# Kernel tuning notes

Hardware: AMD Instinct MI355X
Metric: run time of the kernel (lower is better)

Reference implementation:

```python
import jax, jax.numpy as jnp
import numpy as np

N = 50000      # amino-acid nodes
DIN = 64       # input feature dim
DH = 64        # hidden dim (= GAT out_feats per head)
H = 4          # attention heads
E_RES, E_SEQ, E_KNN = 400000, 100000, 400000
EPS = 1e-5


def setup_inputs() -> dict:
    key = jax.random.key(0)
    ks = iter(jax.random.split(key, 32))
    def nrm(shape, scale=0.1):
        return jax.random.normal(next(ks), shape, dtype=jnp.float32) * scale
    def edges(E):
        s = jax.random.randint(next(ks), (E,), 0, N, dtype=jnp.int32)
        d = jax.random.randint(next(ks), (E,), 0, N, dtype=jnp.int32)
        return s, d
    x = nrm((N, DIN), 1.0)
    src_res, dst_res = edges(E_RES)
    src_seq, dst_seq = edges(E_SEQ)
    src_knn, dst_knn = edges(E_KNN)
    inp = dict(x=x, src_res=src_res, dst_res=dst_res, src_seq=src_seq,
               dst_seq=dst_seq, src_knn=src_knn, dst_knn=dst_knn)
    # layer 0 (in=DIN), layer 1 (in=DH): per-relation stacked GAT params
    inp.update(W0=nrm((3, DIN, H * DH)), al0=nrm((3, H, DH)), ar0=nrm((3, H, DH)),
               b0=nrm((3, H * DH)), rW0=nrm((3, DIN, H * DH)))
    inp.update(W1=nrm((3, DH, H * DH)), al1=nrm((3, H, DH)), ar1=nrm((3, H, DH)),
               b1=nrm((3, H * DH)), rW1=nrm((3, DH, H * DH)))
    inp.update(fcW0=nrm((DH, DH)), fcb0=nrm((DH,)), fcW1=nrm((DH, DH)), fcb1=nrm((DH,)))
    inp.update(g0=jnp.ones((DIN,), jnp.float32), be0=jnp.zeros((DIN,), jnp.float32),
               g1=jnp.ones((DH,), jnp.float32), be1=jnp.zeros((DH,), jnp.float32))
    return inp


def _bn(x, g, b):
    mu = jnp.mean(x, axis=0)
    var = jnp.mean((x - mu) ** 2, axis=0)
    return (x - mu) * jax.lax.rsqrt(var + EPS) * g + b


def _gat(h, src, dst, W, al, ar, bias, rW):
    # DGL GATConv (feat_drop off in eval, residual=True via res_fc Linear, bias)
    n = h.shape[0]
    fs = (h @ W).reshape(n, H, DH)                    # [N,H,D]
    el = jnp.sum(fs * al, axis=-1)                    # [N,H]
    er = jnp.sum(fs * ar, axis=-1)
    e = jax.nn.leaky_relu(el[src] + er[dst], 0.2)     # [E,H]
    m = jax.ops.segment_max(e, dst, num_segments=n)
    a = jnp.exp(e - m[dst])
    s = jax.ops.segment_sum(a, dst, num_segments=n)
    alpha = a / s[dst]                                # edge-softmax per dst/head
    rst = jax.ops.segment_sum(alpha[:, :, None] * fs[src], dst, num_segments=n)
    return rst + (h @ rW).reshape(n, H, DH) + bias.reshape(1, H, DH)


def _layer(x, edges, W, al, ar, b, rW, fcW, fcb, g, be):
    x = _bn(x, g, be)
    h = jnp.zeros((x.shape[0], H, DH), x.dtype)
    for r, (s_, d_) in enumerate(edges):              # 3 relation types, summed
        h = h + _gat(x, s_, d_, W[r], al[r], ar[r], b[r], rW[r])
    x = jnp.mean(h, axis=1)                           # mean over heads
    return jax.nn.relu(x @ fcW + fcb)


def reference(x, src_res, dst_res, src_seq, dst_seq, src_knn, dst_knn,
              W0, al0, ar0, b0, rW0, W1, al1, ar1, b1, rW1,
              fcW0, fcb0, fcW1, fcb1, g0, be0, g1, be1):
    edges = [(src_res, dst_res), (src_seq, dst_seq), (src_knn, dst_knn)]
    x = _layer(x, edges, W0, al0, ar0, b0, rW0, fcW0, fcb0, g0, be0)
    x = _layer(x, edges, W1, al1, ar1, b1, rW1, fcW1, fcb1, g1, be1)
    return x
```

## Files before the change

### kernel.cpp

```cpp
#include <hip/hip_runtime.h>
#include <math.h>

#define NN    50000
#define DD    64
#define HH    4
#define E_RES 400000
#define E_SEQ 100000
#define E_KNN 400000
#define ETOT  (E_RES+E_SEQ+E_KNN)
#define SCH   4096
#define SNB   ((NN + SCH - 1)/SCH)
#define RPS   (NN + 4)
#define MBLK  ((NN+63)/64)
#define NBLK  ((NN+255)/256)
#define ZS    800
#define KTOT  864
#define CTPS  (ETOT + 32)
#define NGRP  (NN/4)
#define AGB   ((3*NGRP)/4)

typedef __attribute__((ext_vector_type(8))) short short8;
typedef __attribute__((ext_vector_type(4))) float floatx4;

__device__ inline unsigned short f2bf(float f){
  union{float f; unsigned u;} v; v.f=f;
  unsigned r = v.u + 0x7FFF + ((v.u>>16)&1);
  return (unsigned short)(r>>16);
}
__device__ inline float bf2f(unsigned short u){
  union{unsigned u; float f;} v; v.u=(unsigned)u<<16; return v.f;
}

__global__ void k_hist3(const int* __restrict__ d0, const int* __restrict__ d1,
                        const int* __restrict__ d2, int* __restrict__ cnt){
  int i = blockIdx.x*256 + threadIdx.x;
  if(i < E_RES)                atomicAdd(&cnt[d0[i]], 1);
  else if(i < E_RES+E_SEQ)     atomicAdd(&cnt[NN + d1[i-E_RES]], 1);
  else if(i < ETOT)            atomicAdd(&cnt[2*NN + d2[i-E_RES-E_SEQ]], 1);
}

__global__ void __launch_bounds__(256)
k_blocksum(const int* __restrict__ hist, int* __restrict__ bsums){
  int r = blockIdx.x / SNB, b = blockIdx.x % SNB;
  const int* cnt = hist + r*NN;
  int t = threadIdx.x;
  int end = min((b+1)*SCH, NN);
  int s = 0;
  for(int j = b*SCH + t; j < end; j += 256) s += cnt[j];
  __shared__ int sh[4];
  for(int off=32; off; off>>=1) s += __shfl_down(s, off, 64);
  int lane = t & 63, w = t >> 6;
  if(lane==0) sh[w]=s;
  __syncthreads();
  if(t==0) bsums[blockIdx.x] = sh[0]+sh[1]+sh[2]+sh[3];
}

__global__ void __launch_bounds__(256)
k_scanwrite(const int* __restrict__ hist, const int* __restrict__ bsums,
            int* __restrict__ rowptr, int* __restrict__ cursor){
  int r = blockIdx.x / SNB, b = blockIdx.x % SNB;
  const int* cnt = hist + r*NN;
  int* rp  = rowptr + r*RPS;
  int* cur = cursor + r*NN;
  __shared__ int sh_off;
  __shared__ int wtot[4];
  int t = threadIdx.x;
  if(t==0){
    int o=0, tot=0;
    for(int i=0;i<SNB;i++){ int v=bsums[r*SNB+i]; if(i<b) o+=v; tot+=v; }
    sh_off=o;
    if(b==0) rp[NN]=tot;
  }
  int base = b*SCH + t*16;
  int v[16];
  bool full = (base+16 <= NN);
  if(full){
    int4 a0=((const int4*)cnt)[base/4+0];
    int4 a1=((const int4*)cnt)[base/4+1];
    int4 a2=((const int4*)cnt)[base/4+2];
    int4 a3=((const int4*)cnt)[base/4+3];
    v[0]=a0.x;v[1]=a0.y;v[2]=a0.z;v[3]=a0.w;
    v[4]=a1.x;v[5]=a1.y;v[6]=a1.z;v[7]=a1.w;
    v[8]=a2.x;v[9]=a2.y;v[10]=a2.z;v[11]=a2.w;
    v[12]=a3.x;v[13]=a3.y;v[14]=a3.z;v[15]=a3.w;
  } else {
    for(int j=0;j<16;j++){ int idx=base+j; v[j]=(idx<NN)?cnt[idx]:0; }
  }
  int loc=0;
  #pragma unroll
  for(int j=0;j<16;j++) loc += v[j];
  int lane = t & 63, w = t >> 6;
  int inc = loc;
  for(int off=1; off<64; off<<=1){ int n=__shfl_up(inc, off, 64); if(lane>=off) inc+=n; }
  if(lane==63) wtot[w]=inc;
  __syncthreads();
  int woff=0;
  for(int i=0;i<w;i++) woff += wtot[i];
  int run = sh_off + woff + inc - loc;
  if(full){
    int o[16];
    #pragma unroll
    for(int j=0;j<16;j++){ o[j]=run; run+=v[j]; }
    ((int4*)rp )[base/4+0]=make_int4(o[0],o[1],o[2],o[3]);
    ((int4*)rp )[base/4+1]=make_int4(o[4],o[5],o[6],o[7]);
    ((int4*)rp )[base/4+2]=make_int4(o[8],o[9],o[10],o[11]);
    ((int4*)rp )[base/4+3]=make_int4(o[12],o[13],o[14],o[15]);
    ((int4*)cur)[base/4+0]=make_int4(o[0],o[1],o[2],o[3]);
    ((int4*)cur)[base/4+1]=make_int4(o[4],o[5],o[6],o[7]);
    ((int4*)cur)[base/4+2]=make_int4(o[8],o[9],o[10],o[11]);
    ((int4*)cur)[base/4+3]=make_int4(o[12],o[13],o[14],o[15]);
  } else {
    for(int j=0;j<16;j++){
      int idx=base+j;
      if(idx<NN){ rp[idx]=run; cur[idx]=run; run+=v[j]; }
    }
  }
}

__global__ void k_scatter3(const int* __restrict__ s0, const int* __restrict__ d0,
                           const int* __restrict__ s1, const int* __restrict__ d1,
                           const int* __restrict__ s2, const int* __restrict__ d2,
                           int* __restrict__ cursor, int* __restrict__ csr){
  int i = blockIdx.x*256 + threadIdx.x;
  if(i < E_RES){
    int pos = atomicAdd(&cursor[d0[i]],1);
    __builtin_nontemporal_store(s0[i], &csr[pos]);
  } else if(i < E_RES+E_SEQ){
    int j=i-E_RES;
    int pos = atomicAdd(&cursor[NN+d1[j]],1);
    __builtin_nontemporal_store(s1[j], &csr[E_RES+pos]);
  } else if(i < ETOT){
    int j=i-E_RES-E_SEQ;
    int pos = atomicAdd(&cursor[2*NN+d2[j]],1);
    __builtin_nontemporal_store(s2[j], &csr[E_RES+E_SEQ+pos]);
  }
}

__global__ void k_bnstats(const float* __restrict__ x, float* __restrict__ stats,
                          unsigned short* __restrict__ Abf){
  __shared__ float sh[512];
  int t = threadIdx.x, col = t & 63, rg = t >> 6;
  float s=0.f, q=0.f;
  for(int row = blockIdx.x*4 + rg; row < NN; row += gridDim.x*4){
    float v = x[(size_t)row*64 + col]; s += v; q += v*v;
    Abf[(size_t)row*64 + col] = f2bf(v);
  }
  sh[t]=s; sh[256+t]=q; __syncthreads();
  if(rg==0){
    s = sh[col]+sh[64+col]+sh[128+col]+sh[192+col];
    q = sh[256+col]+sh[320+col]+sh[384+col]+sh[448+col];
    atomicAdd(&stats[col], s); atomicAdd(&stats[64+col], q);
  }
}

__global__ void __launch_bounds__(256)
k_prep3(const float* __restrict__ stats, const float* __restrict__ g,
        const float* __restrict__ be, const float* __restrict__ W,
        const float* __restrict__ al, const float* __restrict__ ar,
        const float* __restrict__ b, const float* __restrict__ rW,
        const float* __restrict__ fcW, const float* __restrict__ fcb,
        float* __restrict__ wbufF){
  __shared__ float scale[64], shift[64];
  int t = threadIdx.x;
  if(t<64){
    float mu  = stats[t]*(1.0f/NN);
    float var = stats[64+t]*(1.0f/NN) - mu*mu;
    float sc  = g[t]*rsqrtf(var + 1e-5f);
    scale[t]=sc; shift[t]=be[t]-mu*sc;
  }
  __syncthreads();
  char* wb = (char*)wbufF;
  unsigned short* Wf = (unsigned short*)wbufF;
  float* biasF = (float*)(wb + 110592);
  int bid = blockIdx.x;
  if(bid < 52){
    __shared__ float fcWs[4096];
    for(int i=t;i<4096;i+=256) fcWs[i]=fcW[i];
    __syncthreads();
    int j = bid*16 + (t>>4);
    int cg = (t&15)*4;
    float Wrow[64];
    if(j < 64){
      for(int d=0; d<64; d++){
        float w=0.f;
        for(int r=0;r<3;r++)
          #pragma unroll
          for(int h=0;h<4;h++)
            w += rW[((size_t)(r*64+j))*256 + h*64 + d];
        Wrow[d] = scale[j]*0.25f*w;
      }
    } else {
      int jj = j-64;
      int r = jj>>8, dc = jj&255, h = dc&3, c = dc>>2;
      const float* Wp = W + ((size_t)(r*64+c))*256 + h*64;
      float sc = 0.25f*scale[c];
      #pragma unroll
      for(int d=0; d<64; d++) Wrow[d] = sc*Wp[d];
    }
    #pragma unroll
    for(int cc=0; cc<4; cc++){
      int col = cg+cc;
      float acc=0.f;
      #pragma unroll
      for(int d=0; d<64; d++) acc += Wrow[d]*fcWs[d*64+col];
      Wf[(size_t)col*KTOT + j] = f2bf(acc);
    }
  } else if(bid < 58){
    int wv = (bid-52)*4 + (t>>6);
    int r = wv >> 3, cc = wv & 7, h = cc & 3, k = t & 63;
    const float* av = ((cc>=4)?ar:al) + (r*HH+h)*64;
    const float* Wk = W + ((size_t)(r*64+k))*256 + h*64;
    float w=0.f;
    for(int d2=0; d2<64; d2++) w += Wk[d2]*av[d2];
    float* WelR = (float*)(wb + 110848 + r*2080);
    WelR[cc*64 + k] = scale[k]*w;
    float bp = shift[k]*w;
    for(int off=32; off; off>>=1) bp += __shfl_down(bp, off, 64);
    if(k==0) (WelR + 512)[cc] = bp;
  } else {
    __shared__ float S[3][64];
    __shared__ float BH[64];
    if(t<192){
      int r=t>>6, d=t&63;
      float s=0.f;
      #pragma unroll
      for(int h=0;h<4;h++){
        const float* Wp = W + (size_t)(r*64)*256 + h*64 + d;
        for(int k=0;k<64;k++) s += shift[k]*Wp[(size_t)k*256];
      }
      S[r][d]=0.25f*s;
    } else {
      int d = t-192;
      float s=0.f;
      for(int k=0;k<64;k++){
        float w=0.f;
        for(int r=0;r<3;r++)
          #pragma unroll
          for(int h=0;h<4;h++)
            w += rW[((size_t)(r*64+k))*256 + h*64 + d];
        s += shift[k]*0.25f*w;
      }
      float bb=0.f;
      for(int r=0;r<3;r++)
        #pragma unroll
        for(int h=0;h<4;h++) bb += b[r*256 + h*64 + d];
      BH[d] = s + 0.25f*bb;
    }
    __syncthreads();
    if(t<192){
      int r=t>>6, col=t&63;
      float acc=0.f;
      for(int d=0;d<64;d++) acc += S[r][d]*fcW[d*64+col];
      Wf[(size_t)col*KTOT + 832 + r] = f2bf(acc);
    } else {
      int col=t-192;
      float acc=0.f;
      for(int d=0;d<64;d++) acc += BH[d]*fcW[d*64+col];
      biasF[col] = acc + fcb[col];
    }
    if(t<64){
      for(int j=835;j<KTOT;j++) Wf[(size_t)t*KTOT + j] = 0;
    }
  }
}

__global__ void __launch_bounds__(256)
k_el3(const float* __restrict__ A, const float* __restrict__ wbufF,
      float* __restrict__ EL){
  int r = blockIdx.x / NBLK;
  const char* wb = (const char*)wbufF;
  const float* Wel = (const float*)(wb + 110848 + r*2080);
  const float* biasE = Wel + 512;
  float* ELr = EL + (size_t)r*NN*8;
  __shared__ float sw[512];
  __shared__ float sb[8];
  int t = threadIdx.x;
  sw[t]=Wel[t]; sw[256+t]=Wel[256+t];
  if(t<8) sb[t]=biasE[t];
  __syncthreads();
  int n = (blockIdx.x % NBLK)*256 + t;
  if(n>=NN) return;
  float acc[8];
  #pragma unroll
  for(int c=0;c<8;c++) acc[c]=sb[c];
  const float4* Ar = (const float4*)(A + (size_t)n*64);
  #pragma unroll
  for(int kq=0;kq<16;kq++){
    float4 a = Ar[kq];
    #pragma unroll
    for(int c=0;c<8;c++){
      const float* w = sw + c*64 + kq*4;
      acc[c] += a.x*w[0] + a.y*w[1] + a.z*w[2] + a.w*w[3];
    }
  }
  ((float4*)ELr)[n*2]   = make_float4(acc[0],acc[1],acc[2],acc[3]);
  ((float4*)ELr)[n*2+1] = make_float4(acc[4],acc[5],acc[6],acc[7]);
}

__global__ void __launch_bounds__(256)
k_edgecoef3(const float* __restrict__ EL, const int* __restrict__ rowptr,
            const int* __restrict__ csr, unsigned short* __restrict__ coefT){
  int r = blockIdx.x / NBLK;
  const float* ELr = EL + (size_t)r*NN*8;
  const int* rp = rowptr + r*RPS;
  int off = (r==0)?0:(r==1)?E_RES:(E_RES+E_SEQ);
  const int* cs = csr + off;
  unsigned short* t0 = coefT + off;
  unsigned short* t1 = coefT + (size_t)CTPS + off;
  unsigned short* t2 = coefT + (size_t)2*CTPS + off;
  unsigned short* t3 = coefT + (size_t)3*CTPS + off;
  int n = (blockIdx.x % NBLK)*256 + threadIdx.x;
  if(n>=NN) return;
  int beg = rp[n], end = rp[n+1];
  if(end<=beg) return;
  const float4 er = ((const float4*)ELr)[n*2+1];
  float m0=-1e30f,m1=-1e30f,m2=-1e30f,m3=-1e30f;
  float s0=0.f,s1=0.f,s2=0.f,s3=0.f;
  for(int i=beg;i<end;i++){
    int src = cs[i];
    float4 el = ((const float4*)ELr)[src*2];
    float e0=el.x+er.x, e1=el.y+er.y, e2=el.z+er.z, e3=el.w+er.w;
    e0 = e0>0.f? e0 : 0.2f*e0;
    e1 = e1>0.f? e1 : 0.2f*e1;
    e2 = e2>0.f? e2 : 0.2f*e2;
    e3 = e3>0.f? e3 : 0.2f*e3;
    float n0=fmaxf(m0,e0); s0=s0*__expf(m0-n0)+__expf(e0-n0); m0=n0;
    float n1=fmaxf(m1,e1); s1=s1*__expf(m1-n1)+__expf(e1-n1); m1=n1;
    float n2=fmaxf(m2,e2); s2=s2*__expf(m2-n2)+__expf(e2-n2); m2=n2;
    float n3=fmaxf(m3,e3); s3=s3*__expf(m3-n3)+__expf(e3-n3); m3=n3;
  }
  float r0=1.f/s0, r1=1.f/s1, r2=1.f/s2, r3=1.f/s3;
  for(int i=beg;i<end;i++){
    int src = cs[i];
    float4 el = ((const float4*)ELr)[src*2];
    float e0=el.x+er.x, e1=el.y+er.y, e2=el.z+er.z, e3=el.w+er.w;
    e0 = e0>0.f? e0 : 0.2f*e0;
    e1 = e1>0.f? e1 : 0.2f*e1;
    e2 = e2>0.f? e2 : 0.2f*e2;
    e3 = e3>0.f? e3 : 0.2f*e3;
    t0[i] = f2bf(__expf(e0-m0)*r0);
    t1[i] = f2bf(__expf(e1-m1)*r1);
    t2[i] = f2bf(__expf(e2-m2)*r2);
    t3[i] = f2bf(__expf(e3-m3)*r3);
  }
}

__global__ void __launch_bounds__(256)
k_aggzr(const unsigned short* __restrict__ Abf, const int* __restrict__ rowptr,
        const int* __restrict__ csr, const unsigned short* __restrict__ coefT,
        unsigned short* __restrict__ Zbf){
  int w    = blockIdx.x*4 + (threadIdx.x>>6);
  int lane = threadIdx.x & 63;
  int r = w / NGRP;
  int g = w - r*NGRP;
  int n4 = g << 2;
  int m = lane & 15, kq = lane >> 4;
  int nn = m >> 2, h = m & 3;
  const int* rp = rowptr + r*RPS;
  int off = (r==0)?0:(r==1)?E_RES:(E_RES+E_SEQ);
  const int* cs = csr + off;
  const unsigned short* cT = coefT + (size_t)h*CTPS + off;
  int rpn  = rp[n4+nn];
  int rpn1 = rp[n4+nn+1];
  unsigned dg = (unsigned)(rpn1 - rpn);
  int beg = __shfl(rpn, 0, 64);
  int end = __shfl(rpn1, 15, 64);
  floatx4 acc0={0.f,0.f,0.f,0.f};
  floatx4 acc1={0.f,0.f,0.f,0.f};
  floatx4 acc2={0.f,0.f,0.f,0.f};
  floatx4 acc3={0.f,0.f,0.f,0.f};
  for(int eb = (beg & ~31); eb < end; eb += 32){
    int p0 = eb + kq*8;
    union { uint4 q; short8 v; } af;
    af.q = *(const uint4*)(cT + p0);
    int qd = p0 - rpn;
    unsigned w0 = (((unsigned)(qd+0)<dg)?0x0000FFFFu:0u) | (((unsigned)(qd+1)<dg)?0xFFFF0000u:0u);
    unsigned w1 = (((unsigned)(qd+2)<dg)?0x0000FFFFu:0u) | (((unsigned)(qd+3)<dg)?0xFFFF0000u:0u);
    unsigned w2 = (((unsigned)(qd+4)<dg)?0x0000FFFFu:0u) | (((unsigned)(qd+5)<dg)?0xFFFF0000u:0u);
    unsigned w3 = (((unsigned)(qd+6)<dg)?0x0000FFFFu:0u) | (((unsigned)(qd+7)<dg)?0xFFFF0000u:0u);
    af.q.x &= w0; af.q.y &= w1; af.q.z &= w2; af.q.w &= w3;
    const int* csp = cs + p0;
    int s0=csp[0],s1=csp[1],s2=csp[2],s3=csp[3],s4=csp[4],s5=csp[5],s6=csp[6],s7=csp[7];
    const unsigned short* q0 = Abf + ((size_t)s0<<6) + m;
    const unsigned short* q1 = Abf + ((size_t)s1<<6) + m;
    const unsigned short* q2 = Abf + ((size_t)s2<<6) + m;
    const unsigned short* q3 = Abf + ((size_t)s3<<6) + m;
    const unsigned short* q4 = Abf + ((size_t)s4<<6) + m;
    const unsigned short* q5 = Abf + ((size_t)s5<<6) + m;
    const unsigned short* q6 = Abf + ((size_t)s6<<6) + m;
    const unsigned short* q7 = Abf + ((size_t)s7<<6) + m;
    union { unsigned u[4]; short8 v; } b0,b1,b2,b3;
    b0.u[0]=(unsigned)q0[0] |((unsigned)q1[0]<<16);
    b0.u[1]=(unsigned)q2[0] |((unsigned)q3[0]<<16);
    b0.u[2]=(unsigned)q4[0] |((unsigned)q5[0]<<16);
    b0.u[3]=(unsigned)q6[0] |((unsigned)q7[0]<<16);
    b1.u[0]=(unsigned)q0[16]|((unsigned)q1[16]<<16);
    b1.u[1]=(unsigned)q2[16]|((unsigned)q3[16]<<16);
    b1.u[2]=(unsigned)q4[16]|((unsigned)q5[16]<<16);
    b1.u[3]=(unsigned)q6[16]|((unsigned)q7[16]<<16);
    b2.u[0]=(unsigned)q0[32]|((unsigned)q1[32]<<16);
    b2.u[1]=(unsigned)q2[32]|((unsigned)q3[32]<<16);
    b2.u[2]=(unsigned)q4[32]|((unsigned)q5[32]<<16);
    b2.u[3]=(unsigned)q6[32]|((unsigned)q7[32]<<16);
    b3.u[0]=(unsigned)q0[48]|((unsigned)q1[48]<<16);
    b3.u[1]=(unsigned)q2[48]|((unsigned)q3[48]<<16);
    b3.u[2]=(unsigned)q4[48]|((unsigned)q5[48]<<16);
    b3.u[3]=(unsigned)q6[48]|((unsigned)q7[48]<<16);
    acc0 = __builtin_amdgcn_mfma_f32_16x16x32_bf16(af.v, b0.v, acc0, 0,0,0);
    acc1 = __builtin_amdgcn_mfma_f32_16x16x32_bf16(af.v, b1.v, acc1, 0,0,0);
    acc2 = __builtin_amdgcn_mfma_f32_16x16x32_bf16(af.v, b2.v, acc2, 0,0,0);
    acc3 = __builtin_amdgcn_mfma_f32_16x16x32_bf16(af.v, b3.v, acc3, 0,0,0);
  }
  size_t zb = (size_t)(n4 + kq)*ZS + (size_t)r*256 + (size_t)m*4;
  ushort4 o;
  o.x=f2bf(acc0[0]); o.y=f2bf(acc0[1]); o.z=f2bf(acc0[2]); o.w=f2bf(acc0[3]);
  *(ushort4*)(Zbf + zb)       = o;
  o.x=f2bf(acc1[0]); o.y=f2bf(acc1[1]); o.z=f2bf(acc1[2]); o.w=f2bf(acc1[3]);
  *(ushort4*)(Zbf + zb + 64)  = o;
  o.x=f2bf(acc2[0]); o.y=f2bf(acc2[1]); o.z=f2bf(acc2[2]); o.w=f2bf(acc2[3]);
  *(ushort4*)(Zbf + zb + 128) = o;
  o.x=f2bf(acc3[0]); o.y=f2bf(acc3[1]); o.z=f2bf(acc3[2]); o.w=f2bf(acc3[3]);
  *(ushort4*)(Zbf + zb + 192) = o;
  int degk = __shfl((int)dg, kq<<2, 64);
  size_t fb = (size_t)(n4+kq)*ZS + 768;
  if(m==0)
    Zbf[fb + r] = degk>0 ? (unsigned short)0x3F80 : (unsigned short)0;
  if(r==0 && m>=1){
    Zbf[fb + 2 + m] = 0;
    if(m<15) Zbf[fb + 17 + m] = 0;
  }
}

__global__ void __launch_bounds__(256)
k_mfmaZ(const unsigned short* __restrict__ Abf, const unsigned short* __restrict__ Zbf,
        const float* __restrict__ wbufF, float* __restrict__ out,
        unsigned short* __restrict__ Abf2, float* __restrict__ stats, int dostats){
  __shared__ float spart[4][2][32];
  const unsigned short* Wf = (const unsigned short*)wbufF;
  const float* biasF = (const float*)((const char*)wbufF + 110592);
  int t = threadIdx.x, wv = t>>6, lane = t&63, m = lane&15, kq = lane>>4;
  int rt = blockIdx.x >> 1, ch = blockIdx.x & 1;
  int cb = ch*2;
  int row = rt*64 + wv*16 + m;
  int rc = row < NN ? row : NN-1;
  floatx4 acc0 = {0.f,0.f,0.f,0.f};
  floatx4 acc1 = {0.f,0.f,0.f,0.f};
  const unsigned short* Arow = Abf + (size_t)rc*64;
  const unsigned short* Zrow = Zbf + (size_t)rc*ZS;
  #pragma unroll
  for(int kb=0; kb<27; kb++){
    short8 a;
    if(kb<2) a = *(const short8*)(Arow + kb*32 + kq*8);
    else     a = *(const short8*)(Zrow + (kb-2)*32 + kq*8);
    int ko = kb*32 + kq*8;
    short8 b0 = *(const short8*)(Wf + (size_t)((cb+0)*16+m)*KTOT + ko);
    short8 b1 = *(const short8*)(Wf + (size_t)((cb+1)*16+m)*KTOT + ko);
    acc0 = __builtin_amdgcn_mfma_f32_16x16x32_bf16(a, b0, acc0, 0,0,0);
    acc1 = __builtin_amdgcn_mfma_f32_16x16x32_bf16(a, b1, acc1, 0,0,0);
  }
  int orow = rt*64 + wv*16 + kq*4;
  #pragma unroll
  for(int ct=0; ct<2; ct++){
    int col = (cb+ct)*16 + m;
    int lcol = ct*16 + m;
    floatx4 acc = (ct==0)?acc0:acc1;
    float bb = biasF[col];
    float sv=0.f, qv=0.f;
    #pragma unroll
    for(int ri=0; ri<4; ri++){
      int ro = orow + ri;
      if(ro < NN){
        float v = fmaxf(acc[ri] + bb, 0.f);
        out[(size_t)ro*64 + col] = v;
        if(dostats){
          Abf2[(size_t)ro*64 + col] = f2bf(v);
          sv += v; qv += v*v;
        }
      }
    }
    if(dostats){
      sv += __shfl_xor(sv, 16, 64); qv += __shfl_xor(qv, 16, 64);
      sv += __shfl_xor(sv, 32, 64); qv += __shfl_xor(qv, 32, 64);
      if(kq==0){ spart[wv][0][lcol]=sv; spart[wv][1][lcol]=qv; }
    }
  }
  if(dostats){
    __syncthreads();
    if(t<32){
      float s = spart[0][0][t]+spart[1][0][t]+spart[2][0][t]+spart[3][0][t];
      float q = spart[0][1][t]+spart[1][1][t]+spart[2][1][t]+spart[3][1][t];
      atomicAdd(&stats[ch*32+t], s); atomicAdd(&stats[64+ch*32+t], q);
    }
  }
}

extern "C" void kernel_launch(void* const* d_in, const int* in_sizes, int n_in,
                              void* d_out, int out_size, void* d_ws, size_t ws_size,
                              hipStream_t stream){
  const float* x      =(const float*)d_in[0];
  const int* src_res  =(const int*)d_in[1];
  const int* dst_res  =(const int*)d_in[2];
  const int* src_seq  =(const int*)d_in[3];
  const int* dst_seq  =(const int*)d_in[4];
  const int* src_knn  =(const int*)d_in[5];
  const int* dst_knn  =(const int*)d_in[6];
  const float* W0 =(const float*)d_in[7];
  const float* al0=(const float*)d_in[8];
  const float* ar0=(const float*)d_in[9];
  const float* b0 =(const float*)d_in[10];
  const float* rW0=(const float*)d_in[11];
  const float* W1 =(const float*)d_in[12];
  const float* al1=(const float*)d_in[13];
  const float* ar1=(const float*)d_in[14];
  const float* b1 =(const float*)d_in[15];
  const float* rW1=(const float*)d_in[16];
  const float* fcW0=(const float*)d_in[17];
  const float* fcb0=(const float*)d_in[18];
  const float* fcW1=(const float*)d_in[19];
  const float* fcb1=(const float*)d_in[20];
  const float* g0 =(const float*)d_in[21];
  const float* be0=(const float*)d_in[22];
  const float* g1 =(const float*)d_in[23];
  const float* be1=(const float*)d_in[24];

  char* ws=(char*)d_ws;
  int*   hist   =(int*)  (ws+0);
  float* stats0 =(float*)(ws+600000);
  float* stats1 =(float*)(ws+600512);
  int*   rowptr =(int*)  (ws+601024);
  int*   cursor =(int*)  (ws+1201088);
  int*   csr    =(int*)  (ws+1801088);
  float* wbuf   =(float*)(ws+5401088);
  int*   bsums  =(int*)  (ws+5525344);
  unsigned short* Abf  =(unsigned short*)(ws+5526528);
  unsigned short* Zbf  =(unsigned short*)(ws+11926528UL);
  float* xbuf   =(float*)(ws+91926528UL);
  float* EL     =(float*)(ws+104726528UL);
  unsigned short* coefT=(unsigned short*)(ws+109526528UL);
  unsigned short* Abf2 =(unsigned short*)(ws+123926528UL);

  hipMemsetAsync(ws, 0, 601024, stream);

  const int EBLK=(ETOT+255)/256;
  k_hist3<<<EBLK,256,0,stream>>>(dst_res,dst_seq,dst_knn,hist);
  k_blocksum<<<3*SNB,256,0,stream>>>(hist,bsums);
  k_scanwrite<<<3*SNB,256,0,stream>>>(hist,bsums,rowptr,cursor);
  k_scatter3<<<EBLK,256,0,stream>>>(src_res,dst_res,src_seq,dst_seq,
                                    src_knn,dst_knn,cursor,csr);

  k_bnstats<<<256,256,0,stream>>>(x,stats0,Abf);
  k_prep3<<<59,256,0,stream>>>(stats0,g0,be0,W0,al0,ar0,b0,rW0,fcW0,fcb0,wbuf);
  k_el3<<<3*NBLK,256,0,stream>>>(x,wbuf,EL);
  k_edgecoef3<<<3*NBLK,256,0,stream>>>(EL,rowptr,csr,coefT);
  k_aggzr<<<AGB,256,0,stream>>>(Abf,rowptr,csr,coefT,Zbf);
  k_mfmaZ<<<2*MBLK,256,0,stream>>>(Abf,Zbf,wbuf,xbuf,Abf2,stats1,1);
  k_prep3<<<59,256,0,stream>>>(stats1,g1,be1,W1,al1,ar1,b1,rW1,fcW1,fcb1,wbuf);
  k_el3<<<3*NBLK,256,0,stream>>>(xbuf,wbuf,EL);
  k_edgecoef3<<<3*NBLK,256,0,stream>>>(EL,rowptr,csr,coefT);
  k_aggzr<<<AGB,256,0,stream>>>(Abf2,rowptr,csr,coefT,Zbf);
  k_mfmaZ<<<2*MBLK,256,0,stream>>>(Abf2,Zbf,wbuf,(float*)d_out,Abf2,stats0,0);
}
```

Baseline: 510.0 us.

## Build CSR via two-level bucket partition with shared-memory atomics

Replaces the per-node global-atomic histogram, scan and scatter with a two-pass bucket sort. Edges are first counted and partitioned into coarse 512-node buckets per relation using shared-memory counters. Each bucket is then locally histogrammed, scanned and scattered in shared memory to produce rowptr and csr. This aims to cut contended global atomics and random global writes during CSR construction. The cost is an extra packed-pairs pass through a buffer that aliases Zbf, and it relies on src and rank values fitting in 16 bits.

```diff
diff --git a/kernel.cpp b/kernel.cpp
--- a/kernel.cpp
+++ b/kernel.cpp
@@ -8,8 +8,6 @@
 #define E_SEQ 100000
 #define E_KNN 400000
 #define ETOT  (E_RES+E_SEQ+E_KNN)
-#define SCH   4096
-#define SNB   ((NN + SCH - 1)/SCH)
 #define RPS   (NN + 4)
 #define MBLK  ((NN+63)/64)
 #define NBLK  ((NN+255)/256)
@@ -18,6 +16,10 @@
 #define CTPS  (ETOT + 32)
 #define NGRP  (NN/4)
 #define AGB   ((3*NGRP)/4)
+#define NBUK  98
+#define TBUK  (3*NBUK)
+#define EPB   4096
+#define PABLK ((ETOT+EPB-1)/EPB)
 
 typedef __attribute__((ext_vector_type(8))) short short8;
 typedef __attribute__((ext_vector_type(4))) float floatx4;
@@ -31,108 +33,118 @@
   union{unsigned u; float f;} v; v.u=(unsigned)u<<16; return v.f;
 }
 
-__global__ void k_hist3(const int* __restrict__ d0, const int* __restrict__ d1,
-                        const int* __restrict__ d2, int* __restrict__ cnt){
-  int i = blockIdx.x*256 + threadIdx.x;
-  if(i < E_RES)                atomicAdd(&cnt[d0[i]], 1);
-  else if(i < E_RES+E_SEQ)     atomicAdd(&cnt[NN + d1[i-E_RES]], 1);
-  else if(i < ETOT)            atomicAdd(&cnt[2*NN + d2[i-E_RES-E_SEQ]], 1);
-}
-
-__global__ void __launch_bounds__(256)
-k_blocksum(const int* __restrict__ hist, int* __restrict__ bsums){
-  int r = blockIdx.x / SNB, b = blockIdx.x % SNB;
-  const int* cnt = hist + r*NN;
+
+__global__ void __launch_bounds__(256)
+k_bucketcnt(const int* __restrict__ d0, const int* __restrict__ d1,
+            const int* __restrict__ d2, int* __restrict__ bcnt){
+  __shared__ int cnt[TBUK];
   int t = threadIdx.x;
-  int end = min((b+1)*SCH, NN);
-  int s = 0;
-  for(int j = b*SCH + t; j < end; j += 256) s += cnt[j];
-  __shared__ int sh[4];
-  for(int off=32; off; off>>=1) s += __shfl_down(s, off, 64);
-  int lane = t & 63, w = t >> 6;
-  if(lane==0) sh[w]=s;
-  __syncthreads();
-  if(t==0) bsums[blockIdx.x] = sh[0]+sh[1]+sh[2]+sh[3];
-}
-
-__global__ void __launch_bounds__(256)
-k_scanwrite(const int* __restrict__ hist, const int* __restrict__ bsums,
-            int* __restrict__ rowptr, int* __restrict__ cursor){
-  int r = blockIdx.x / SNB, b = blockIdx.x % SNB;
-  const int* cnt = hist + r*NN;
-  int* rp  = rowptr + r*RPS;
-  int* cur = cursor + r*NN;
-  __shared__ int sh_off;
-  __shared__ int wtot[4];
+  for(int i=t;i<TBUK;i+=256) cnt[i]=0;
+  __syncthreads();
+  int ebase = blockIdx.x*EPB;
+  #pragma unroll
+  for(int j=0;j<16;j++){
+    int i = ebase + j*256 + t;
+    int d, r;
+    if(i < E_RES){ d=d0[i]; r=0; }
+    else if(i < E_RES+E_SEQ){ d=d1[i-E_RES]; r=1; }
+    else if(i < ETOT){ d=d2[i-E_RES-E_SEQ]; r=2; }
+    else continue;
+    atomicAdd(&cnt[r*NBUK + (d>>9)], 1);
+  }
+  __syncthreads();
+  for(int i=t;i<TBUK;i+=256){ int c=cnt[i]; if(c) atomicAdd(&bcnt[i], c); }
+}
+
+__global__ void k_bucketscan(const int* __restrict__ bcnt,
+                             int* __restrict__ bbase, int* __restrict__ bcur){
+  __shared__ int sh[TBUK];
   int t = threadIdx.x;
-  if(t==0){
-    int o=0, tot=0;
-    for(int i=0;i<SNB;i++){ int v=bsums[r*SNB+i]; if(i<b) o+=v; tot+=v; }
-    sh_off=o;
-    if(b==0) rp[NN]=tot;
-  }
-  int base = b*SCH + t*16;
-  int v[16];
-  bool full = (base+16 <= NN);
-  if(full){
-    int4 a0=((const int4*)cnt)[base/4+0];
-    int4 a1=((const int4*)cnt)[base/4+1];
-    int4 a2=((const int4*)cnt)[base/4+2];
-    int4 a3=((const int4*)cnt)[base/4+3];
-    v[0]=a0.x;v[1]=a0.y;v[2]=a0.z;v[3]=a0.w;
-    v[4]=a1.x;v[5]=a1.y;v[6]=a1.z;v[7]=a1.w;
-    v[8]=a2.x;v[9]=a2.y;v[10]=a2.z;v[11]=a2.w;
-    v[12]=a3.x;v[13]=a3.y;v[14]=a3.z;v[15]=a3.w;
-  } else {
-    for(int j=0;j<16;j++){ int idx=base+j; v[j]=(idx<NN)?cnt[idx]:0; }
-  }
-  int loc=0;
-  #pragma unroll
-  for(int j=0;j<16;j++) loc += v[j];
-  int lane = t & 63, w = t >> 6;
-  int inc = loc;
-  for(int off=1; off<64; off<<=1){ int n=__shfl_up(inc, off, 64); if(lane>=off) inc+=n; }
-  if(lane==63) wtot[w]=inc;
-  __syncthreads();
-  int woff=0;
-  for(int i=0;i<w;i++) woff += wtot[i];
-  int run = sh_off + woff + inc - loc;
-  if(full){
-    int o[16];
-    #pragma unroll
-    for(int j=0;j<16;j++){ o[j]=run; run+=v[j]; }
-    ((int4*)rp )[base/4+0]=make_int4(o[0],o[1],o[2],o[3]);
-    ((int4*)rp )[base/4+1]=make_int4(o[4],o[5],o[6],o[7]);
-    ((int4*)rp )[base/4+2]=make_int4(o[8],o[9],o[10],o[11]);
-    ((int4*)rp )[base/4+3]=make_int4(o[12],o[13],o[14],o[15]);
-    ((int4*)cur)[base/4+0]=make_int4(o[0],o[1],o[2],o[3]);
-    ((int4*)cur)[base/4+1]=make_int4(o[4],o[5],o[6],o[7]);
-    ((int4*)cur)[base/4+2]=make_int4(o[8],o[9],o[10],o[11]);
-    ((int4*)cur)[base/4+3]=make_int4(o[12],o[13],o[14],o[15]);
-  } else {
-    for(int j=0;j<16;j++){
-      int idx=base+j;
-      if(idx<NN){ rp[idx]=run; cur[idx]=run; run+=v[j]; }
-    }
-  }
-}
-
-__global__ void k_scatter3(const int* __restrict__ s0, const int* __restrict__ d0,
-                           const int* __restrict__ s1, const int* __restrict__ d1,
-                           const int* __restrict__ s2, const int* __restrict__ d2,
-                           int* __restrict__ cursor, int* __restrict__ csr){
-  int i = blockIdx.x*256 + threadIdx.x;
-  if(i < E_RES){
-    int pos = atomicAdd(&cursor[d0[i]],1);
-    __builtin_nontemporal_store(s0[i], &csr[pos]);
-  } else if(i < E_RES+E_SEQ){
-    int j=i-E_RES;
-    int pos = atomicAdd(&cursor[NN+d1[j]],1);
-    __builtin_nontemporal_store(s1[j], &csr[E_RES+pos]);
-  } else if(i < ETOT){
-    int j=i-E_RES-E_SEQ;
-    int pos = atomicAdd(&cursor[2*NN+d2[j]],1);
-    __builtin_nontemporal_store(s2[j], &csr[E_RES+E_SEQ+pos]);
+  if(t < 64){
+    int carry = 0;
+    for(int c=0;c<5;c++){
+      int idx = c*64 + t;
+      int v = (idx < TBUK) ? bcnt[idx] : 0;
+      int inc = v;
+      for(int off=1; off<64; off<<=1){ int n=__shfl_up(inc, off, 64); if(t>=off) inc+=n; }
+      if(idx < TBUK) sh[idx] = carry + inc - v;
+      carry += __shfl(inc, 63, 64);
+    }
+  }
+  __syncthreads();
+  if(t < TBUK){ bbase[t] = sh[t]; bcur[t] = sh[t]; }
+  if(t == 0) bbase[TBUK] = ETOT;
+}
+
+__global__ void __launch_bounds__(256)
+k_partA(const int* __restrict__ s0, const int* __restrict__ d0,
+        const int* __restrict__ s1, const int* __restrict__ d1,
+        const int* __restrict__ s2, const int* __restrict__ d2,
+        int* __restrict__ bcur, unsigned* __restrict__ pairs){
+  __shared__ int cnt[TBUK];
+  __shared__ int gb[TBUK];
+  int t = threadIdx.x;
+  for(int i=t;i<TBUK;i+=256) cnt[i]=0;
+  __syncthreads();
+  int ebase = blockIdx.x*EPB;
+  unsigned meta[16], pk[16];
+  #pragma unroll
+  for(int j=0;j<16;j++){
+    int i = ebase + j*256 + t;
+    int s, d, r;
+    if(i < E_RES){ s=s0[i]; d=d0[i]; r=0; }
+    else if(i < E_RES+E_SEQ){ int k=i-E_RES; s=s1[k]; d=d1[k]; r=1; }
+    else if(i < ETOT){ int k=i-E_RES-E_SEQ; s=s2[k]; d=d2[k]; r=2; }
+    else { meta[j]=0xFFFFFFFFu; continue; }
+    int bk = r*NBUK + (d>>9);
+    int rk = atomicAdd(&cnt[bk], 1);
+    meta[j] = ((unsigned)bk<<16) | (unsigned)rk;
+    pk[j]   = ((unsigned)(d&511)<<16) | (unsigned)s;
+  }
+  __syncthreads();
+  for(int i=t;i<TBUK;i+=256){ int c=cnt[i]; gb[i] = c ? atomicAdd(&bcur[i], c) : 0; }
+  __syncthreads();
+  #pragma unroll
+  for(int j=0;j<16;j++){
+    unsigned mt = meta[j];
+    if(mt != 0xFFFFFFFFu)
+      pairs[gb[mt>>16] + (mt & 0xFFFFu)] = pk[j];
+  }
+}
+
+__global__ void __launch_bounds__(256)
+k_partB(const unsigned* __restrict__ pairs, const int* __restrict__ bbase,
+        int* __restrict__ rowptr, int* __restrict__ csr){
+  int bb = blockIdx.x, r = bb / NBUK, b = bb - r*NBUK;
+  int dbase = b*512, dmax = min(512, NN - dbase);
+  int off = (r==0)?0:(r==1)?E_RES:(E_RES+E_SEQ);
+  __shared__ int hist[512];
+  __shared__ int curs[513];
+  int t = threadIdx.x;
+  hist[t]=0; hist[256+t]=0;
+  __syncthreads();
+  int beg = bbase[bb], end = bbase[bb+1];
+  for(int i=beg+t; i<end; i+=256) atomicAdd(&hist[pairs[i]>>16], 1);
+  __syncthreads();
+  if(t < 64){
+    int carry = 0;
+    for(int c=0;c<8;c++){
+      int v = hist[c*64+t];
+      int inc = v;
+      for(int o2=1; o2<64; o2<<=1){ int n=__shfl_up(inc, o2, 64); if(t>=o2) inc+=n; }
+      curs[c*64+t] = (beg - off) + carry + inc - v;
+      carry += __shfl(inc, 63, 64);
+    }
+    if(t==0) curs[512] = end - off;
+  }
+  __syncthreads();
+  int* rp = rowptr + r*RPS + dbase;
+  for(int i=t; i<=dmax; i+=256) rp[i] = curs[i];
+  __syncthreads();
+  for(int i=beg+t; i<end; i+=256){
+    unsigned p = pairs[i];
+    int pos = atomicAdd(&curs[p>>16], 1);
+    csr[off + pos] = (int)(p & 0xFFFFu);
   }
 }
 
@@ -524,16 +536,17 @@
   const float* be1=(const float*)d_in[24];
 
   char* ws=(char*)d_ws;
-  int*   hist   =(int*)  (ws+0);
+  int*   bcnt   =(int*)  (ws+0);
+  int*   bbase  =(int*)  (ws+4096);
   float* stats0 =(float*)(ws+600000);
   float* stats1 =(float*)(ws+600512);
   int*   rowptr =(int*)  (ws+601024);
-  int*   cursor =(int*)  (ws+1201088);
+  int*   bcur   =(int*)  (ws+1201088);
   int*   csr    =(int*)  (ws+1801088);
   float* wbuf   =(float*)(ws+5401088);
-  int*   bsums  =(int*)  (ws+5525344);
   unsigned short* Abf  =(unsigned short*)(ws+5526528);
   unsigned short* Zbf  =(unsigned short*)(ws+11926528UL);
+  unsigned* pairs =(unsigned*)(ws+11926528UL);
   float* xbuf   =(float*)(ws+91926528UL);
   float* EL     =(float*)(ws+104726528UL);
   unsigned short* coefT=(unsigned short*)(ws+109526528UL);
@@ -541,12 +554,11 @@
 
   hipMemsetAsync(ws, 0, 601024, stream);
 
-  const int EBLK=(ETOT+255)/256;
-  k_hist3<<<EBLK,256,0,stream>>>(dst_res,dst_seq,dst_knn,hist);
-  k_blocksum<<<3*SNB,256,0,stream>>>(hist,bsums);
-  k_scanwrite<<<3*SNB,256,0,stream>>>(hist,bsums,rowptr,cursor);
-  k_scatter3<<<EBLK,256,0,stream>>>(src_res,dst_res,src_seq,dst_seq,
-                                    src_knn,dst_knn,cursor,csr);
+  k_bucketcnt<<<PABLK,256,0,stream>>>(dst_res,dst_seq,dst_knn,bcnt);
+  k_bucketscan<<<1,512,0,stream>>>(bcnt,bbase,bcur);
+  k_partA<<<PABLK,256,0,stream>>>(src_res,dst_res,src_seq,dst_seq,
+                                  src_knn,dst_knn,bcur,pairs);
+  k_partB<<<TBUK,256,0,stream>>>(pairs,bbase,rowptr,csr);
 
   k_bnstats<<<256,256,0,stream>>>(x,stats0,Abf);
   k_prep3<<<59,256,0,stream>>>(stats0,g0,be0,W0,al0,ar0,b0,rW0,fcW0,fcb0,wbuf);
```

Measured after the change: 436.2 us. 14.5% less time.
